# Kernel tuning notes

Hardware: AMD Instinct MI355X
Metric: run time of the kernel (lower is better)

Reference implementation:

```python
import jax, jax.numpy as jnp
import numpy as np
from jax import lax

D_MODEL = 512
D_STATE = 16
D_CONV = 4
DT_RANK = 32  # ceil(512/16)
BATCH = 4
SEQ = 2048
FN = 32


def setup_inputs() -> dict:
    key = jax.random.key(0)
    ks = jax.random.split(key, 12)
    s = 0.02
    d, n, r = D_MODEL, D_STATE, DT_RANK
    return {
        "atoms": jax.random.normal(ks[0], (BATCH, SEQ, d), jnp.float32),
        # normalized "adjacency"-like matrix so delta_p = dis_dense @ delta stays O(1)
        "dis_dense": jax.random.uniform(ks[1], (BATCH, SEQ, SEQ), jnp.float32) / SEQ,
        "gpt_emb": jax.random.normal(ks[2], (BATCH, d), jnp.float32),
        "fg_emb": jax.random.normal(ks[3], (BATCH, FN, d), jnp.float32),
        "in_proj_w": jax.random.normal(ks[4], (2 * d, d), jnp.float32) * s,
        "conv_w": jax.random.normal(ks[5], (d, 1, D_CONV), jnp.float32) * s,  # depthwise OIW
        "conv_b": jnp.zeros((d,), jnp.float32),
        "x_proj_w": jax.random.normal(ks[6], (r + 2 * n, d), jnp.float32) * s,
        "dt_proj_w": jax.random.normal(ks[7], (d, r), jnp.float32) * s,
        "dt_proj_b": jnp.full((d,), 0.5, jnp.float32),
        "A_log": jnp.log(jnp.broadcast_to(jnp.arange(1, n + 1, dtype=jnp.float32), (d, n))),
        "D_param": jnp.ones((d,), jnp.float32),
        "out_proj_w": jax.random.normal(ks[8], (d, d), jnp.float32) * s,
        "film_w1": jax.random.normal(ks[9], (d, d), jnp.float32) * s,
        "film_b1": jnp.zeros((d,), jnp.float32),
        "film_w2": jax.random.normal(ks[10], (2 * d, d), jnp.float32) * s,
        "film_b2": jnp.zeros((2 * d,), jnp.float32),
    }


def reference(atoms, dis_dense, gpt_emb, fg_emb,
              in_proj_w, conv_w, conv_b, x_proj_w, dt_proj_w, dt_proj_b,
              A_log, D_param, out_proj_w, film_w1, film_b1, film_w2, film_b2):
    b, l, d = atoms.shape
    n = A_log.shape[1]

    # --- CrossAttentionFusion: Q=atoms, K/V=fg_emb ---
    scores = jnp.einsum('bld,bfd->blf', atoms, fg_emb) / (d ** 0.5)
    attn = jax.nn.softmax(scores, axis=-1)
    x = atoms + jnp.einsum('blf,bfd->bld', attn, fg_emb)

    # --- FiLM modulation from gpt_emb ---
    h = jax.nn.silu(gpt_emb @ film_w1.T + film_b1)
    gamma, beta = jnp.split(h @ film_w2.T + film_b2, 2, axis=-1)
    x = x * gamma[:, None, :] + beta[:, None, :]

    # --- in_proj and split into (x, res) ---
    xs, res = jnp.split(x @ in_proj_w.T, 2, axis=-1)

    # --- depthwise causal-padded conv1d, truncate to l ---
    xc = jnp.transpose(xs, (0, 2, 1))  # [b, d, l]
    xc = lax.conv_general_dilated(xc, conv_w, window_strides=(1,),
                                  padding=[(D_CONV - 1, D_CONV - 1)],
                                  feature_group_count=d)[:, :, :l]
    xc = xc + conv_b[None, :, None]
    u = jax.nn.silu(jnp.transpose(xc, (0, 2, 1)))  # [b, l, d]

    # --- SSM ---
    A = -jnp.exp(A_log)                      # [d, n]
    x_dbl = u @ x_proj_w.T                   # [b, l, r+2n]
    delta, Bm, Cm = jnp.split(x_dbl, [DT_RANK, DT_RANK + n], axis=-1)
    delta = jax.nn.softplus(delta @ dt_proj_w.T + dt_proj_b)  # [b, l, d]
    delta_p = jnp.einsum('blk,bkd->bld', dis_dense, delta)     # graph-mixed delta

    deltaA = jnp.exp(delta_p[..., None] * A)                   # [b, l, d, n]
    deltaB_u = delta_p[..., None] * Bm[:, :, None, :] * u[..., None]  # [b, l, d, n]

    def step(carry, inp):
        dA_t, dBu_t, C_t = inp
        carry = dA_t * carry + dBu_t                # [b, d, n]
        y_t = jnp.einsum('bdn,bn->bd', carry, C_t)
        return carry, y_t

    init = jnp.zeros((b, d, n), deltaA.dtype)
    _, ys = lax.scan(step, init,
                     (jnp.moveaxis(deltaA, 1, 0),
                      jnp.moveaxis(deltaB_u, 1, 0),
                      jnp.moveaxis(Cm, 1, 0)))
    y = jnp.moveaxis(ys, 0, 1) + u * D_param       # [b, l, d]

    # --- gate, out_proj, nonfinite -> 0 ---
    y = y * jax.nn.silu(res)
    out = y @ out_proj_w.T
    return jnp.where(jnp.isfinite(out), out, 0.0)
```

## Files before the change

kernel.cpp:

```cpp
#include <hip/hip_runtime.h>
#include <stdint.h>

#define D_MODEL 512
#define D_STATE 16
#define DT_RANK 32
#define SEQ 2048
#define NBATCH 4
#define FN 32
#define CHUNK 16
#define NCHUNK 128
#define DPPLANE ((size_t)8192*D_MODEL)

typedef unsigned short u16;
using s16x8 = __attribute__((ext_vector_type(8))) short;
using f32x4 = __attribute__((ext_vector_type(4))) float;
using f32x8 = __attribute__((ext_vector_type(8))) float;
using bf16x8 = __attribute__((ext_vector_type(8))) __bf16;

typedef __attribute__((address_space(3))) void lds_void;
typedef __attribute__((address_space(1))) const void glb_void;

__device__ __forceinline__ void gload16(const void* g, void* l) {
  __builtin_amdgcn_global_load_lds((glb_void*)g, (lds_void*)l, 16, 0, 0);
}

__device__ inline u16 f2bf(float f) {
  uint32_t u = __float_as_uint(f);
  u += 0x7FFFu + ((u >> 16) & 1u);
  return (u16)(u >> 16);
}

__device__ __forceinline__ s16x8 pack8bf(float4 lo, float4 hi) {
  f32x8 v;
  v[0] = lo.x; v[1] = lo.y; v[2] = lo.z; v[3] = lo.w;
  v[4] = hi.x; v[5] = hi.y; v[6] = hi.z; v[7] = hi.w;
  bf16x8 b = __builtin_convertvector(v, bf16x8);
  return __builtin_bit_cast(s16x8, b);
}

__global__ __launch_bounds__(256) void film1_kernel(
    const float* __restrict__ gpt, const float* __restrict__ w1,
    const float* __restrict__ b1, float* __restrict__ h)
{
  int b = blockIdx.y, r0 = blockIdx.x*16, t = threadIdx.x;
  __shared__ float g[D_MODEL];
  for (int i = t; i < D_MODEL; i += 256) g[i] = gpt[b*D_MODEL + i];
  __syncthreads();
  int r = r0 + (t >> 4), ln = t & 15;
  const float* wr = &w1[(size_t)r*D_MODEL + ln*32];
  const float* gg = &g[ln*32];
  float s = 0.f;
  #pragma unroll
  for (int k = 0; k < 32; k += 4) {
    float4 w = *(const float4*)&wr[k];
    s += w.x*gg[k] + w.y*gg[k+1] + w.z*gg[k+2] + w.w*gg[k+3];
  }
  s += __shfl_down(s, 8); s += __shfl_down(s, 4);
  s += __shfl_down(s, 2); s += __shfl_down(s, 1);
  if (ln == 0) { float v = s + b1[r]; h[b*D_MODEL + r] = v / (1.f + expf(-v)); }
}

__global__ __launch_bounds__(256) void film2_kernel(
    const float* __restrict__ h, const float* __restrict__ w2,
    const float* __restrict__ b2, float* __restrict__ gb)
{
  int b = blockIdx.y, r0 = blockIdx.x*16, t = threadIdx.x;
  __shared__ float hs[D_MODEL];
  for (int i = t; i < D_MODEL; i += 256) hs[i] = h[b*D_MODEL + i];
  __syncthreads();
  int r = r0 + (t >> 4), ln = t & 15;
  const float* wr = &w2[(size_t)r*D_MODEL + ln*32];
  const float* gg = &hs[ln*32];
  float s = 0.f;
  #pragma unroll
  for (int k = 0; k < 32; k += 4) {
    float4 w = *(const float4*)&wr[k];
    s += w.x*gg[k] + w.y*gg[k+1] + w.z*gg[k+2] + w.w*gg[k+3];
  }
  s += __shfl_down(s, 8); s += __shfl_down(s, 4);
  s += __shfl_down(s, 2); s += __shfl_down(s, 1);
  if (ln == 0) gb[b*1024 + r] = s + b2[r];
}

__global__ __launch_bounds__(256) void build_fgpad_kernel(
    const float* __restrict__ fg, u16* __restrict__ fgpad)
{
  int row = blockIdx.x & 127, b = blockIdx.x >> 7, t = threadIdx.x;
  u16* dst = &fgpad[((size_t)b*128 + row)*D_MODEL];
  if (row < FN) {
    const float* src = &fg[((size_t)b*FN + row)*D_MODEL];
    float2 v = *(const float2*)&src[t*2];
    dst[t*2] = f2bf(v.x); dst[t*2+1] = f2bf(v.y);
  } else {
    dst[t*2] = 0; dst[t*2+1] = 0;
  }
}

__global__ __launch_bounds__(256) void softmax_kernel(
    const float* __restrict__ scores, float* __restrict__ attn)
{
  int wave = threadIdx.x >> 6, lane = threadIdx.x & 63;
  int row = blockIdx.x*4 + wave;
  float s = scores[(size_t)row*128 + (lane & 31)] * 0.04419417382415922f;
  float m = s;
  #pragma unroll
  for (int o = 16; o; o >>= 1) m = fmaxf(m, __shfl_xor(m, o));
  float e = __expf(s - m);
  float sum = e;
  #pragma unroll
  for (int o = 16; o; o >>= 1) sum += __shfl_xor(sum, o);
  if (lane < 32) attn[(size_t)row*FN + lane] = e / sum;
}

__global__ __launch_bounds__(256) void pv_film_kernel(
    const float* __restrict__ atoms, const float* __restrict__ fg,
    const float* __restrict__ attn, const float* __restrict__ gb,
    u16* __restrict__ xout)
{
  int wave = threadIdx.x >> 6, lane = threadIdx.x & 63;
  int row = blockIdx.x*4 + wave;
  int b = row >> 11;
  int d0 = lane*8;
  const float* arow = &atoms[(size_t)row*D_MODEL + d0];
  float4 acc0 = *(const float4*)&arow[0];
  float4 acc1 = *(const float4*)&arow[4];
  const float* attn_row = &attn[(size_t)row*FN];
  const float* fgb = &fg[(size_t)b*FN*D_MODEL + d0];
  #pragma unroll 8
  for (int f = 0; f < FN; f++) {
    float w = attn_row[f];
    float4 g0 = *(const float4*)&fgb[(size_t)f*D_MODEL];
    float4 g1 = *(const float4*)&fgb[(size_t)f*D_MODEL + 4];
    acc0.x += w*g0.x; acc0.y += w*g0.y; acc0.z += w*g0.z; acc0.w += w*g0.w;
    acc1.x += w*g1.x; acc1.y += w*g1.y; acc1.z += w*g1.z; acc1.w += w*g1.w;
  }
  const float* gbg = &gb[(size_t)b*1024 + d0];
  float4 gm0 = *(const float4*)&gbg[0];
  float4 gm1 = *(const float4*)&gbg[4];
  float4 bt0 = *(const float4*)&gbg[D_MODEL];
  float4 bt1 = *(const float4*)&gbg[D_MODEL + 4];
  s16x8 o;
  o[0] = (short)f2bf(acc0.x*gm0.x + bt0.x);
  o[1] = (short)f2bf(acc0.y*gm0.y + bt0.y);
  o[2] = (short)f2bf(acc0.z*gm0.z + bt0.z);
  o[3] = (short)f2bf(acc0.w*gm0.w + bt0.w);
  o[4] = (short)f2bf(acc1.x*gm1.x + bt1.x);
  o[5] = (short)f2bf(acc1.y*gm1.y + bt1.y);
  o[6] = (short)f2bf(acc1.z*gm1.z + bt1.z);
  o[7] = (short)f2bf(acc1.w*gm1.w + bt1.w);
  *(s16x8*)&xout[(size_t)row*D_MODEL + d0] = o;
}

__global__ __launch_bounds__(256) void cvt_bf16_kernel(
    const float* __restrict__ in, u16* __restrict__ out, int n4)
{
  int i = blockIdx.x*256 + threadIdx.x;
  if (i >= n4) return;
  float4 v = *(const float4*)&in[(size_t)i*4];
  ushort4 o; o.x = f2bf(v.x); o.y = f2bf(v.y); o.z = f2bf(v.z); o.w = f2bf(v.w);
  *(ushort4*)&out[(size_t)i*4] = o;
}

__global__ __launch_bounds__(256) void build_wcomb_kernel(
    const float* __restrict__ dtw, const float* __restrict__ xpw, u16* __restrict__ w)
{
  int row = blockIdx.x, t = threadIdx.x;
  if (row < D_MODEL) {
    __shared__ float dr[DT_RANK];
    if (t < DT_RANK) dr[t] = dtw[row*DT_RANK + t];
    __syncthreads();
    for (int k = t; k < D_MODEL; k += 256) {
      float s = 0.f;
      #pragma unroll
      for (int r = 0; r < DT_RANK; r++) s += dr[r] * xpw[r*D_MODEL + k];
      w[(size_t)row*D_MODEL + k] = f2bf(s);
    }
  } else if (row < D_MODEL + 32) {
    for (int k = t; k < D_MODEL; k += 256)
      w[(size_t)row*D_MODEL + k] = f2bf(xpw[(size_t)(DT_RANK + row - D_MODEL)*D_MODEL + k]);
  } else {
    for (int k = t; k < D_MODEL; k += 256)
      w[(size_t)row*D_MODEL + k] = 0;
  }
}

__global__ __launch_bounds__(256) void gemm_bt64_kernel(
    const u16* __restrict__ A, const u16* __restrict__ B, float* __restrict__ C,
    int M, int N, int K, int clampFinite)
{
  int gx = gridDim.x, gy = gridDim.y;
  int flat = blockIdx.x + gx*blockIdx.y;
  int cpx = (gx*gy) >> 3;
  flat = (flat & 7)*cpx + (flat >> 3);
  int bx = flat % gx, by = flat / gx;
  int m0 = by * 64, n0 = bx * 128;
  __shared__ u16 As[64][32];
  __shared__ u16 Bs[128][32];
  int tid = threadIdx.x, lane = tid & 63, wave = tid >> 6;
  int wm = (wave >> 1) * 32, wn = (wave & 1) * 64;
  int fr = lane & 15, fk = (lane >> 4) * 8;
  int srow = tid >> 2, scol = (tid & 3) * 8;
  f32x4 acc[2][4] = {};
  for (int k0 = 0; k0 < K; k0 += 32) {
    gload16(&A[(size_t)(m0 + srow)*K + k0 + scol],      &As[srow][scol]);
    gload16(&B[(size_t)(n0 + srow)*K + k0 + scol],      &Bs[srow][scol]);
    gload16(&B[(size_t)(n0 + 64 + srow)*K + k0 + scol], &Bs[64 + srow][scol]);
    __syncthreads();
    s16x8 af[2], bf[4];
    #pragma unroll
    for (int i = 0; i < 2; i++) af[i] = *(const s16x8*)(&As[wm + i*16 + fr][fk]);
    #pragma unroll
    for (int i = 0; i < 4; i++) bf[i] = *(const s16x8*)(&Bs[wn + i*16 + fr][fk]);
    #pragma unroll
    for (int mi = 0; mi < 2; mi++)
      #pragma unroll
      for (int ni = 0; ni < 4; ni++)
        acc[mi][ni] = __builtin_amdgcn_mfma_f32_16x16x32_bf16(af[mi], bf[ni], acc[mi][ni], 0, 0, 0);
    __syncthreads();
  }
  int cr = (lane >> 4) * 4, cc = lane & 15;
  #pragma unroll
  for (int mi = 0; mi < 2; mi++)
    #pragma unroll
    for (int ni = 0; ni < 4; ni++) {
      int rowb = m0 + wm + mi*16 + cr, col = n0 + wn + ni*16 + cc;
      #pragma unroll
      for (int r = 0; r < 4; r++) {
        float v = acc[mi][ni][r];
        if (clampFinite && !isfinite(v)) v = 0.f;
        C[(size_t)(rowb + r)*N + col] = v;
      }
    }
}

__global__ __launch_bounds__(256) void gemm_f32a_kernel(
    const float* __restrict__ Ag, const u16* __restrict__ Bg, float* __restrict__ Cg,
    int M, int N, int K, long long azs, long long bzs, long long czs,
    int clampFinite, int swz)
{
  int gx = gridDim.x, gy = gridDim.y;
  int flat = blockIdx.x + gx*(blockIdx.y + gy*blockIdx.z);
  if (swz) {
    int cpx = (gx*gy*(int)gridDim.z) >> 3;
    flat = (flat & 7)*cpx + (flat >> 3);
  }
  int bx = flat % gx, tmp = flat / gx;
  int by = tmp % gy, bz = tmp / gy;
  const float* A = Ag + (size_t)bz * azs;
  const u16* B = Bg + (size_t)bz * bzs;
  float* C = Cg + (size_t)bz * czs;
  int m0 = by * 128, n0 = bx * 128;
  __shared__ u16 As[128][32];
  __shared__ u16 Bs[128][32];
  int tid = threadIdx.x, lane = tid & 63, wave = tid >> 6;
  int wm = (wave >> 1) * 64, wn = (wave & 1) * 64;
  int fr = lane & 15, fk = (lane >> 4) * 8;
  int srow = tid >> 2, scol = (tid & 3) * 8;
  f32x4 acc[4][4] = {};
  for (int k0 = 0; k0 < K; k0 += 32) {
    const float* a0p = &A[(size_t)(m0 + srow)*K + k0 + scol];
    const float* a1p = &A[(size_t)(m0 + 64 + srow)*K + k0 + scol];
    float4 a00 = *(const float4*)&a0p[0];
    float4 a01 = *(const float4*)&a0p[4];
    float4 a10 = *(const float4*)&a1p[0];
    float4 a11 = *(const float4*)&a1p[4];
    gload16(&B[(size_t)(n0 + srow)*K + k0 + scol],      &Bs[srow][scol]);
    gload16(&B[(size_t)(n0 + 64 + srow)*K + k0 + scol], &Bs[64 + srow][scol]);
    *(s16x8*)&As[srow][scol]      = pack8bf(a00, a01);
    *(s16x8*)&As[64 + srow][scol] = pack8bf(a10, a11);
    __syncthreads();
    s16x8 af[4], bf[4];
    #pragma unroll
    for (int i = 0; i < 4; i++) af[i] = *(const s16x8*)(&As[wm + i*16 + fr][fk]);
    #pragma unroll
    for (int i = 0; i < 4; i++) bf[i] = *(const s16x8*)(&Bs[wn + i*16 + fr][fk]);
    #pragma unroll
    for (int mi = 0; mi < 4; mi++)
      #pragma unroll
      for (int ni = 0; ni < 4; ni++)
        acc[mi][ni] = __builtin_amdgcn_mfma_f32_16x16x32_bf16(af[mi], bf[ni], acc[mi][ni], 0, 0, 0);
    __syncthreads();
  }
  int cr = (lane >> 4) * 4, cc = lane & 15;
  #pragma unroll
  for (int mi = 0; mi < 4; mi++)
    #pragma unroll
    for (int ni = 0; ni < 4; ni++) {
      int rowb = m0 + wm + mi*16 + cr, col = n0 + wn + ni*16 + cc;
      #pragma unroll
      for (int r = 0; r < 4; r++) {
        float v = acc[mi][ni][r];
        if (clampFinite && !isfinite(v)) v = 0.f;
        C[(size_t)(rowb + r)*N + col] = v;
      }
    }
}

__global__ __launch_bounds__(256) void gemm_dp_splitk_kernel(
    const float* __restrict__ dis, const u16* __restrict__ deltaT,
    float* __restrict__ dpp)
{
  int gx = gridDim.x, gy = gridDim.y;
  int flat = blockIdx.x + gx*(blockIdx.y + gy*blockIdx.z);
  int cpx = (gx*gy*(int)gridDim.z) >> 3;
  flat = (flat & 7)*cpx + (flat >> 3);
  int bx = flat % gx, tmp = flat / gx;
  int by = tmp % gy, bz = tmp / gy;
  int b = bz >> 2, ks = bz & 3;
  const float* A = dis    + (size_t)b*SEQ*SEQ     + ks*512;
  const u16*  B = deltaT  + (size_t)b*D_MODEL*SEQ + ks*512;
  float*      C = dpp     + (size_t)ks*DPPLANE    + (size_t)b*SEQ*D_MODEL;
  int m0 = by * 128, n0 = bx * 128;
  __shared__ u16 As[128][32];
  __shared__ u16 Bs[128][32];
  int tid = threadIdx.x, lane = tid & 63, wave = tid >> 6;
  int wm = (wave >> 1) * 64, wn = (wave & 1) * 64;
  int fr = lane & 15, fk = (lane >> 4) * 8;
  int srow = tid >> 2, scol = (tid & 3) * 8;
  f32x4 acc[4][4] = {};
  for (int k0 = 0; k0 < 512; k0 += 32) {
    const float* a0p = &A[(size_t)(m0 + srow)*SEQ + k0 + scol];
    const float* a1p = &A[(size_t)(m0 + 64 + srow)*SEQ + k0 + scol];
    float4 a00 = *(const float4*)&a0p[0];
    float4 a01 = *(const float4*)&a0p[4];
    float4 a10 = *(const float4*)&a1p[0];
    float4 a11 = *(const float4*)&a1p[4];
    gload16(&B[(size_t)(n0 + srow)*SEQ + k0 + scol],      &Bs[srow][scol]);
    gload16(&B[(size_t)(n0 + 64 + srow)*SEQ + k0 + scol], &Bs[64 + srow][scol]);
    *(s16x8*)&As[srow][scol]      = pack8bf(a00, a01);
    *(s16x8*)&As[64 + srow][scol] = pack8bf(a10, a11);
    __syncthreads();
    s16x8 af[4], bf[4];
    #pragma unroll
    for (int i = 0; i < 4; i++) af[i] = *(const s16x8*)(&As[wm + i*16 + fr][fk]);
    #pragma unroll
    for (int i = 0; i < 4; i++) bf[i] = *(const s16x8*)(&Bs[wn + i*16 + fr][fk]);
    #pragma unroll
    for (int mi = 0; mi < 4; mi++)
      #pragma unroll
      for (int ni = 0; ni < 4; ni++)
        acc[mi][ni] = __builtin_amdgcn_mfma_f32_16x16x32_bf16(af[mi], bf[ni], acc[mi][ni], 0, 0, 0);
    __syncthreads();
  }
  int cr = (lane >> 4) * 4, cc = lane & 15;
  #pragma unroll
  for (int mi = 0; mi < 4; mi++)
    #pragma unroll
    for (int ni = 0; ni < 4; ni++) {
      int rowb = m0 + wm + mi*16 + cr, col = n0 + wn + ni*16 + cc;
      #pragma unroll
      for (int r = 0; r < 4; r++)
        C[(size_t)(rowb + r)*D_MODEL + col] = acc[mi][ni][r];
    }
}

__global__ __launch_bounds__(256) void gemm_delta_kernel(
    const u16* __restrict__ A, const u16* __restrict__ B,
    const float* __restrict__ dtb, u16* __restrict__ deltaT,
    float* __restrict__ Bv, float* __restrict__ Cv)
{
  int gx = gridDim.x, gy = gridDim.y;
  int flat = blockIdx.x + gx*blockIdx.y;
  int cpx = (gx*gy) >> 3;
  flat = (flat & 7)*cpx + (flat >> 3);
  int bx = flat % gx, by = flat / gx;
  int m0 = by * 64, n0 = bx * 128;
  __shared__ u16 As[64][32];
  __shared__ u16 Bs[128][32];
  int tid = threadIdx.x, lane = tid & 63, wave = tid >> 6;
  int wm = (wave >> 1) * 32, wn = (wave & 1) * 64;
  int fr = lane & 15, fk = (lane >> 4) * 8;
  int srow = tid >> 2, scol = (tid & 3) * 8;
  f32x4 acc[2][4] = {};
  for (int k0 = 0; k0 < D_MODEL; k0 += 32) {
    gload16(&A[(size_t)(m0 + srow)*D_MODEL + k0 + scol],      &As[srow][scol]);
    gload16(&B[(size_t)(n0 + srow)*D_MODEL + k0 + scol],      &Bs[srow][scol]);
    gload16(&B[(size_t)(n0 + 64 + srow)*D_MODEL + k0 + scol], &Bs[64 + srow][scol]);
    __syncthreads();
    s16x8 af[2], bf[4];
    #pragma unroll
    for (int i = 0; i < 2; i++) af[i] = *(const s16x8*)(&As[wm + i*16 + fr][fk]);
    #pragma unroll
    for (int i = 0; i < 4; i++) bf[i] = *(const s16x8*)(&Bs[wn + i*16 + fr][fk]);
    #pragma unroll
    for (int mi = 0; mi < 2; mi++)
      #pragma unroll
      for (int ni = 0; ni < 4; ni++)
        acc[mi][ni] = __builtin_amdgcn_mfma_f32_16x16x32_bf16(af[mi], bf[ni], acc[mi][ni], 0, 0, 0);
    __syncthreads();
  }
  int cr = (lane >> 4) * 4, cc = lane & 15;
  #pragma unroll
  for (int mi = 0; mi < 2; mi++)
    #pragma unroll
    for (int ni = 0; ni < 4; ni++) {
      int rowb = m0 + wm + mi*16 + cr, col = n0 + wn + ni*16 + cc;
      if (col < D_MODEL) {
        float bias = dtb[col];
        #pragma unroll
        for (int r = 0; r < 4; r++) {
          float v = acc[mi][ni][r] + bias;
          v = (v > 20.f) ? v : log1pf(expf(v));
          int gr = rowb + r;
          deltaT[((size_t)(gr >> 11)*D_MODEL + col)*SEQ + (gr & (SEQ-1))] = f2bf(v);
        }
      } else if (col < D_MODEL + 16) {
        #pragma unroll
        for (int r = 0; r < 4; r++)
          Bv[(size_t)(rowb + r)*D_STATE + (col - D_MODEL)] = acc[mi][ni][r];
      } else if (col < D_MODEL + 32) {
        #pragma unroll
        for (int r = 0; r < 4; r++)
          Cv[(size_t)(rowb + r)*D_STATE + (col - D_MODEL - 16)] = acc[mi][ni][r];
      }
    }
}

__global__ __launch_bounds__(256) void conv_silu_kernel(
    const float* __restrict__ xsres, const float* __restrict__ cw,
    const float* __restrict__ cb, float* __restrict__ u, u16* __restrict__ ubf)
{
  int idx = blockIdx.x*256 + threadIdx.x;
  int d = (idx & 127) * 4;
  int row = idx >> 7;
  int l = row & (SEQ - 1);
  float w[4][4];
  #pragma unroll
  for (int c = 0; c < 4; c++) *(float4*)w[c] = *(const float4*)&cw[(d + c)*4];
  float4 acc = *(const float4*)&cb[d];
  #pragma unroll
  for (int k = 0; k < 4; k++) {
    int li = l - 3 + k;
    if (li >= 0) {
      float4 v = *(const float4*)&xsres[(size_t)(row - 3 + k)*1024 + d];
      acc.x += v.x*w[0][k]; acc.y += v.y*w[1][k];
      acc.z += v.z*w[2][k]; acc.w += v.w*w[3][k];
    }
  }
  float4 o;
  o.x = acc.x/(1.f+expf(-acc.x)); o.y = acc.y/(1.f+expf(-acc.y));
  o.z = acc.z/(1.f+expf(-acc.z)); o.w = acc.w/(1.f+expf(-acc.w));
  *(float4*)&u[(size_t)row*D_MODEL + d] = o;
  ushort4 ob;
  ob.x = f2bf(o.x); ob.y = f2bf(o.y); ob.z = f2bf(o.z); ob.w = f2bf(o.w);
  *(ushort4*)&ubf[(size_t)row*D_MODEL + d] = ob;
}

__global__ __launch_bounds__(256) void scanA_kernel(
    float* __restrict__ dpp, const float* __restrict__ u,
    const float* __restrict__ Bv, const float* __restrict__ A_log,
    float* __restrict__ slocal, float* __restrict__ sumdp_out)
{
  int d = blockIdx.x*256 + threadIdx.x;
  int c = blockIdx.y, b = blockIdx.z;
  __shared__ float Bs[CHUNK][D_STATE];
  int t = threadIdx.x;
  size_t lbase = (size_t)b*SEQ + c*CHUNK;
  Bs[t >> 4][t & 15] = Bv[(lbase + (t >> 4))*D_STATE + (t & 15)];
  float a[D_STATE];
  #pragma unroll
  for (int n = 0; n < D_STATE; n += 4) {
    float4 v = *(const float4*)&A_log[(size_t)d*D_STATE + n];
    a[n] = -expf(v.x); a[n+1] = -expf(v.y); a[n+2] = -expf(v.z); a[n+3] = -expf(v.w);
  }
  __syncthreads();
  float s[D_STATE];
  #pragma unroll
  for (int n = 0; n < D_STATE; n++) s[n] = 0.f;
  float sd = 0.f;
  for (int j = 0; j < CHUNK; j++) {
    size_t r = lbase + j;
    size_t idx = r*D_MODEL + d;
    float dpv = dpp[idx] + dpp[idx + DPPLANE] + dpp[idx + 2*DPPLANE] + dpp[idx + 3*DPPLANE];
    dpp[idx] = dpv;
    float uv  = u[idx];
    sd += dpv;
    float dbu = dpv * uv;
    #pragma unroll
    for (int n = 0; n < D_STATE; n++)
      s[n] = __expf(a[n]*dpv)*s[n] + dbu*Bs[j][n];
  }
  size_t obase = ((size_t)b*NCHUNK + c)*D_MODEL + d;
  #pragma unroll
  for (int n = 0; n < D_STATE; n += 4)
    *(float4*)&slocal[obase*D_STATE + n] = make_float4(s[n], s[n+1], s[n+2], s[n+3]);
  sumdp_out[obase] = sd;
}

__global__ __launch_bounds__(256) void scanB_kernel(
    const float* __restrict__ slocal, const float* __restrict__ sumdp,
    const float* __restrict__ A_log, float* __restrict__ sIn)
{
  int g = blockIdx.x*256 + threadIdx.x;
  int n = g & 15, d = (g >> 4) & (D_MODEL - 1), b = g >> 13;
  float a = -expf(A_log[d*D_STATE + n]);
  float s = 0.f;
  for (int c = 0; c < NCHUNK; c++) {
    size_t idx = ((size_t)b*NCHUNK + c)*D_MODEL + d;
    sIn[idx*D_STATE + n] = s;
    s = __expf(a * sumdp[idx]) * s + slocal[idx*D_STATE + n];
  }
}

__global__ __launch_bounds__(256) void scanC_kernel(
    const float* __restrict__ dp, const float* __restrict__ u,
    const float* __restrict__ Bv, const float* __restrict__ Cv,
    const float* __restrict__ A_log, const float* __restrict__ Dp,
    const float* __restrict__ xsres, const float* __restrict__ sIn,
    u16* __restrict__ yout)
{
  int d = blockIdx.x*256 + threadIdx.x;
  int c = blockIdx.y, b = blockIdx.z;
  __shared__ float Bs[CHUNK][D_STATE];
  __shared__ float Cs[CHUNK][D_STATE];
  int t = threadIdx.x;
  size_t lbase = (size_t)b*SEQ + c*CHUNK;
  Bs[t >> 4][t & 15] = Bv[(lbase + (t >> 4))*D_STATE + (t & 15)];
  Cs[t >> 4][t & 15] = Cv[(lbase + (t >> 4))*D_STATE + (t & 15)];
  float a[D_STATE];
  #pragma unroll
  for (int n = 0; n < D_STATE; n += 4) {
    float4 v = *(const float4*)&A_log[(size_t)d*D_STATE + n];
    a[n] = -expf(v.x); a[n+1] = -expf(v.y); a[n+2] = -expf(v.z); a[n+3] = -expf(v.w);
  }
  float s[D_STATE];
  size_t ibase = (((size_t)b*NCHUNK + c)*D_MODEL + d)*D_STATE;
  #pragma unroll
  for (int n = 0; n < D_STATE; n += 4) {
    float4 v = *(const float4*)&sIn[ibase + n];
    s[n] = v.x; s[n+1] = v.y; s[n+2] = v.z; s[n+3] = v.w;
  }
  float dparam = Dp[d];
  __syncthreads();
  for (int j = 0; j < CHUNK; j++) {
    size_t r = lbase + j;
    float dpv = dp[r*D_MODEL + d];
    float uv  = u[r*D_MODEL + d];
    float dbu = dpv * uv;
    float y = 0.f;
    #pragma unroll
    for (int n = 0; n < D_STATE; n++) {
      s[n] = __expf(a[n]*dpv)*s[n] + dbu*Bs[j][n];
      y += s[n]*Cs[j][n];
    }
    y += uv * dparam;
    float rr = xsres[r*1024 + D_MODEL + d];
    y *= rr/(1.f + __expf(-rr));
    yout[r*D_MODEL + d] = f2bf(y);
  }
}

extern "C" void kernel_launch(void* const* d_in, const int* in_sizes, int n_in,
                              void* d_out, int out_size, void* d_ws, size_t ws_size,
                              hipStream_t stream)
{
  const float* atoms  = (const float*)d_in[0];
  const float* dis    = (const float*)d_in[1];
  const float* gpt    = (const float*)d_in[2];
  const float* fg     = (const float*)d_in[3];
  const float* inw    = (const float*)d_in[4];
  const float* convw  = (const float*)d_in[5];
  const float* convb  = (const float*)d_in[6];
  const float* xpw    = (const float*)d_in[7];
  const float* dtw    = (const float*)d_in[8];
  const float* dtb    = (const float*)d_in[9];
  const float* A_log  = (const float*)d_in[10];
  const float* Dparam = (const float*)d_in[11];
  const float* outw   = (const float*)d_in[12];
  const float* fw1    = (const float*)d_in[13];
  const float* fb1    = (const float*)d_in[14];
  const float* fw2    = (const float*)d_in[15];
  const float* fb2    = (const float*)d_in[16];

  char* ws = (char*)d_ws;
  size_t off = 0;
  auto alloc = [&](size_t bytes) { char* p = ws + off; off += (bytes + 255) & ~255ull; return p; };
  float* gb     = (float*)alloc((size_t)NBATCH*1024*4);
  float* hbuf   = (float*)alloc((size_t)NBATCH*512*4);
  float* attnb  = (float*)alloc((size_t)8192*FN*4);
  u16*   fgpad  = (u16*)  alloc((size_t)NBATCH*128*512*2);
  float* scores = (float*)alloc((size_t)NBATCH*2048*128*4);
  u16*   xbf    = (u16*)  alloc((size_t)8192*512*2);
  u16*   inwbf  = (u16*)  alloc((size_t)1024*512*2);
  u16*   outwbf = (u16*)  alloc((size_t)512*512*2);
  u16*   wcomb  = (u16*)  alloc((size_t)640*512*2);
  float* xsres  = (float*)alloc((size_t)8192*1024*4);
  float* dpp    = (float*)alloc(4*DPPLANE*4);
  float* ubuf   = (float*)alloc((size_t)8192*512*4);
  u16*   ubf    = (u16*)  alloc((size_t)8192*512*2);
  float* Bv     = (float*)alloc((size_t)8192*16*4);
  float* Cv     = (float*)alloc((size_t)8192*16*4);
  u16*   deltaT = (u16*)  alloc((size_t)NBATCH*512*2048*2);
  float* slocal = (float*)alloc((size_t)NBATCH*NCHUNK*512*16*4);
  float* sumdp  = (float*)alloc((size_t)NBATCH*NCHUNK*512*4);
  float* sIn    = (float*)alloc((size_t)NBATCH*NCHUNK*512*16*4);

  film1_kernel<<<dim3(32, NBATCH), 256, 0, stream>>>(gpt, fw1, fb1, hbuf);
  film2_kernel<<<dim3(64, NBATCH), 256, 0, stream>>>(hbuf, fw2, fb2, gb);

  build_fgpad_kernel<<<NBATCH*128, 256, 0, stream>>>(fg, fgpad);
  gemm_f32a_kernel<<<dim3(1, 2048/128, NBATCH), 256, 0, stream>>>(
      atoms, fgpad, scores, 2048, 128, 512,
      (long long)2048*512, (long long)128*512, (long long)2048*128, 0, 1);
  softmax_kernel<<<8192/4, 256, 0, stream>>>(scores, attnb);
  pv_film_kernel<<<8192/4, 256, 0, stream>>>(atoms, fg, attnb, gb, xbf);

  cvt_bf16_kernel<<<(1024*512/4)/256, 256, 0, stream>>>(inw, inwbf, 1024*512/4);
  cvt_bf16_kernel<<<(512*512/4)/256, 256, 0, stream>>>(outw, outwbf, 512*512/4);
  build_wcomb_kernel<<<640, 256, 0, stream>>>(dtw, xpw, wcomb);

  gemm_bt64_kernel<<<dim3(1024/128, 8192/64), 256, 0, stream>>>(
      xbf, inwbf, xsres, 8192, 1024, 512, 0);
  conv_silu_kernel<<<8192*128/256, 256, 0, stream>>>(xsres, convw, convb, ubuf, ubf);

  gemm_delta_kernel<<<dim3(640/128, 8192/64), 256, 0, stream>>>(
      ubf, wcomb, dtb, deltaT, Bv, Cv);

  gemm_dp_splitk_kernel<<<dim3(512/128, 2048/128, NBATCH*4), 256, 0, stream>>>(
      dis, deltaT, dpp);

  scanA_kernel<<<dim3(2, NCHUNK, NBATCH), 256, 0, stream>>>(dpp, ubuf, Bv, A_log, slocal, sumdp);
  scanB_kernel<<<32768/256, 256, 0, stream>>>(slocal, sumdp, A_log, sIn);
  u16* ybf = xbf;
  scanC_kernel<<<dim3(2, NCHUNK, NBATCH), 256, 0, stream>>>(dpp, ubuf, Bv, Cv, A_log, Dparam, xsres, sIn, ybf);

  gemm_bt64_kernel<<<dim3(512/128, 8192/64), 256, 0, stream>>>(
      ybf, outwbf, (float*)d_out, 8192, 512, 512, 1);
}
```

Measured before the change: 269.1 us.

## Double-buffer LDS tiles in bf16 GEMM and split-K delta GEMM kernels

Adds ping-pong shared-memory buffers to two GEMM kernels so the next K-tile is prefetched (via global_load_lds and register loads) while MFMAs run on the current tile. This removes one of the two barriers per iteration and overlaps global-load latency with compute. In exchange it doubles LDS use per block, which may reduce occupancy, and adds register pressure for the prefetched float4 values in the split-K kernel.

```diff
diff --git a/kernel.cpp b/kernel.cpp
--- a/kernel.cpp
+++ b/kernel.cpp
@@ -194,29 +194,41 @@
   flat = (flat & 7)*cpx + (flat >> 3);
   int bx = flat % gx, by = flat / gx;
   int m0 = by * 64, n0 = bx * 128;
-  __shared__ u16 As[64][32];
-  __shared__ u16 Bs[128][32];
+  __shared__ u16 As[2][64][32];
+  __shared__ u16 Bs[2][128][32];
   int tid = threadIdx.x, lane = tid & 63, wave = tid >> 6;
   int wm = (wave >> 1) * 32, wn = (wave & 1) * 64;
   int fr = lane & 15, fk = (lane >> 4) * 8;
   int srow = tid >> 2, scol = (tid & 3) * 8;
+  const u16* abase  = &A[(size_t)(m0 + srow)*K + scol];
+  const u16* b0base = &B[(size_t)(n0 + srow)*K + scol];
+  const u16* b1base = &B[(size_t)(n0 + 64 + srow)*K + scol];
+  gload16(abase,  &As[0][srow][scol]);
+  gload16(b0base, &Bs[0][srow][scol]);
+  gload16(b1base, &Bs[0][64 + srow][scol]);
+  __syncthreads();
   f32x4 acc[2][4] = {};
-  for (int k0 = 0; k0 < K; k0 += 32) {
-    gload16(&A[(size_t)(m0 + srow)*K + k0 + scol],      &As[srow][scol]);
-    gload16(&B[(size_t)(n0 + srow)*K + k0 + scol],      &Bs[srow][scol]);
-    gload16(&B[(size_t)(n0 + 64 + srow)*K + k0 + scol], &Bs[64 + srow][scol]);
-    __syncthreads();
+  int NT = K >> 5, cur = 0;
+  for (int t = 0; t < NT; t++) {
+    int nxt = cur ^ 1;
+    if (t + 1 < NT) {
+      int k0 = (t + 1) << 5;
+      gload16(&abase[k0],  &As[nxt][srow][scol]);
+      gload16(&b0base[k0], &Bs[nxt][srow][scol]);
+      gload16(&b1base[k0], &Bs[nxt][64 + srow][scol]);
+    }
     s16x8 af[2], bf[4];
     #pragma unroll
-    for (int i = 0; i < 2; i++) af[i] = *(const s16x8*)(&As[wm + i*16 + fr][fk]);
-    #pragma unroll
-    for (int i = 0; i < 4; i++) bf[i] = *(const s16x8*)(&Bs[wn + i*16 + fr][fk]);
+    for (int i = 0; i < 2; i++) af[i] = *(const s16x8*)(&As[cur][wm + i*16 + fr][fk]);
+    #pragma unroll
+    for (int i = 0; i < 4; i++) bf[i] = *(const s16x8*)(&Bs[cur][wn + i*16 + fr][fk]);
     #pragma unroll
     for (int mi = 0; mi < 2; mi++)
       #pragma unroll
       for (int ni = 0; ni < 4; ni++)
         acc[mi][ni] = __builtin_amdgcn_mfma_f32_16x16x32_bf16(af[mi], bf[ni], acc[mi][ni], 0, 0, 0);
     __syncthreads();
+    cur = nxt;
   }
   int cr = (lane >> 4) * 4, cc = lane & 15;
   #pragma unroll
@@ -311,36 +323,58 @@
   const u16*  B = deltaT  + (size_t)b*D_MODEL*SEQ + ks*512;
   float*      C = dpp     + (size_t)ks*DPPLANE    + (size_t)b*SEQ*D_MODEL;
   int m0 = by * 128, n0 = bx * 128;
-  __shared__ u16 As[128][32];
-  __shared__ u16 Bs[128][32];
+  __shared__ u16 As[2][128][32];
+  __shared__ u16 Bs[2][128][32];
   int tid = threadIdx.x, lane = tid & 63, wave = tid >> 6;
   int wm = (wave >> 1) * 64, wn = (wave & 1) * 64;
   int fr = lane & 15, fk = (lane >> 4) * 8;
   int srow = tid >> 2, scol = (tid & 3) * 8;
+  const float* a0base = &A[(size_t)(m0 + srow)*SEQ + scol];
+  const float* a1base = &A[(size_t)(m0 + 64 + srow)*SEQ + scol];
+  const u16* b0base = &B[(size_t)(n0 + srow)*SEQ + scol];
+  const u16* b1base = &B[(size_t)(n0 + 64 + srow)*SEQ + scol];
+  {
+    float4 a00 = *(const float4*)&a0base[0];
+    float4 a01 = *(const float4*)&a0base[4];
+    float4 a10 = *(const float4*)&a1base[0];
+    float4 a11 = *(const float4*)&a1base[4];
+    gload16(b0base, &Bs[0][srow][scol]);
+    gload16(b1base, &Bs[0][64 + srow][scol]);
+    *(s16x8*)&As[0][srow][scol]      = pack8bf(a00, a01);
+    *(s16x8*)&As[0][64 + srow][scol] = pack8bf(a10, a11);
+  }
+  __syncthreads();
   f32x4 acc[4][4] = {};
-  for (int k0 = 0; k0 < 512; k0 += 32) {
-    const float* a0p = &A[(size_t)(m0 + srow)*SEQ + k0 + scol];
-    const float* a1p = &A[(size_t)(m0 + 64 + srow)*SEQ + k0 + scol];
-    float4 a00 = *(const float4*)&a0p[0];
-    float4 a01 = *(const float4*)&a0p[4];
-    float4 a10 = *(const float4*)&a1p[0];
-    float4 a11 = *(const float4*)&a1p[4];
-    gload16(&B[(size_t)(n0 + srow)*SEQ + k0 + scol],      &Bs[srow][scol]);
-    gload16(&B[(size_t)(n0 + 64 + srow)*SEQ + k0 + scol], &Bs[64 + srow][scol]);
-    *(s16x8*)&As[srow][scol]      = pack8bf(a00, a01);
-    *(s16x8*)&As[64 + srow][scol] = pack8bf(a10, a11);
-    __syncthreads();
+  int cur = 0;
+  for (int t = 0; t < 16; t++) {
+    int nxt = cur ^ 1;
+    float4 n00, n01, n10, n11;
+    bool pf = (t + 1 < 16);
+    if (pf) {
+      int k0 = (t + 1) << 5;
+      n00 = *(const float4*)&a0base[k0];
+      n01 = *(const float4*)&a0base[k0 + 4];
+      n10 = *(const float4*)&a1base[k0];
+      n11 = *(const float4*)&a1base[k0 + 4];
+      gload16(&b0base[k0], &Bs[nxt][srow][scol]);
+      gload16(&b1base[k0], &Bs[nxt][64 + srow][scol]);
+    }
     s16x8 af[4], bf[4];
     #pragma unroll
-    for (int i = 0; i < 4; i++) af[i] = *(const s16x8*)(&As[wm + i*16 + fr][fk]);
-    #pragma unroll
-    for (int i = 0; i < 4; i++) bf[i] = *(const s16x8*)(&Bs[wn + i*16 + fr][fk]);
+    for (int i = 0; i < 4; i++) af[i] = *(const s16x8*)(&As[cur][wm + i*16 + fr][fk]);
+    #pragma unroll
+    for (int i = 0; i < 4; i++) bf[i] = *(const s16x8*)(&Bs[cur][wn + i*16 + fr][fk]);
     #pragma unroll
     for (int mi = 0; mi < 4; mi++)
       #pragma unroll
       for (int ni = 0; ni < 4; ni++)
         acc[mi][ni] = __builtin_amdgcn_mfma_f32_16x16x32_bf16(af[mi], bf[ni], acc[mi][ni], 0, 0, 0);
+    if (pf) {
+      *(s16x8*)&As[nxt][srow][scol]      = pack8bf(n00, n01);
+      *(s16x8*)&As[nxt][64 + srow][scol] = pack8bf(n10, n11);
+    }
     __syncthreads();
+    cur = nxt;
   }
   int cr = (lane >> 4) * 4, cc = lane & 15;
   #pragma unroll
```

New measurement: 266.7 us. About the same (-0.9%).

## Pre-convert dis matrix to bf16 and double-buffer LDS tiles in bt64 GEMM

Applied to the files above, without the earlier changes.

Adds a separate conversion pass that turns the fp32 dis_dense matrix into bf16, so the split-K delta-mixing GEMM can load both operands straight into LDS with async global-to-LDS loads instead of loading fp32 and packing in registers. The bf16 copy reuses the slocal scratch buffer, which is only about half the size needed, so it relies on the following sumdp and sIn allocations being contiguous and not yet in use. Separately, the bt64 GEMM gets double-buffered LDS tiles with a prologue load, so the next K-tile is fetched while MFMAs run on the current one. The conversion pass adds a full extra read and write of the large dis tensor, which may outweigh the cheaper GEMM loads.

```diff
diff --git a/kernel.cpp b/kernel.cpp
--- a/kernel.cpp
+++ b/kernel.cpp
@@ -194,29 +194,41 @@
   flat = (flat & 7)*cpx + (flat >> 3);
   int bx = flat % gx, by = flat / gx;
   int m0 = by * 64, n0 = bx * 128;
-  __shared__ u16 As[64][32];
-  __shared__ u16 Bs[128][32];
+  __shared__ u16 As[2][64][32];
+  __shared__ u16 Bs[2][128][32];
   int tid = threadIdx.x, lane = tid & 63, wave = tid >> 6;
   int wm = (wave >> 1) * 32, wn = (wave & 1) * 64;
   int fr = lane & 15, fk = (lane >> 4) * 8;
   int srow = tid >> 2, scol = (tid & 3) * 8;
+  const u16* abase  = &A[(size_t)(m0 + srow)*K + scol];
+  const u16* b0base = &B[(size_t)(n0 + srow)*K + scol];
+  const u16* b1base = &B[(size_t)(n0 + 64 + srow)*K + scol];
+  gload16(abase,  &As[0][srow][scol]);
+  gload16(b0base, &Bs[0][srow][scol]);
+  gload16(b1base, &Bs[0][64 + srow][scol]);
+  __syncthreads();
   f32x4 acc[2][4] = {};
-  for (int k0 = 0; k0 < K; k0 += 32) {
-    gload16(&A[(size_t)(m0 + srow)*K + k0 + scol],      &As[srow][scol]);
-    gload16(&B[(size_t)(n0 + srow)*K + k0 + scol],      &Bs[srow][scol]);
-    gload16(&B[(size_t)(n0 + 64 + srow)*K + k0 + scol], &Bs[64 + srow][scol]);
-    __syncthreads();
+  int NT = K >> 5, cur = 0;
+  for (int t = 0; t < NT; t++) {
+    int nxt = cur ^ 1;
+    if (t + 1 < NT) {
+      int k0 = (t + 1) << 5;
+      gload16(&abase[k0],  &As[nxt][srow][scol]);
+      gload16(&b0base[k0], &Bs[nxt][srow][scol]);
+      gload16(&b1base[k0], &Bs[nxt][64 + srow][scol]);
+    }
     s16x8 af[2], bf[4];
     #pragma unroll
-    for (int i = 0; i < 2; i++) af[i] = *(const s16x8*)(&As[wm + i*16 + fr][fk]);
-    #pragma unroll
-    for (int i = 0; i < 4; i++) bf[i] = *(const s16x8*)(&Bs[wn + i*16 + fr][fk]);
+    for (int i = 0; i < 2; i++) af[i] = *(const s16x8*)(&As[cur][wm + i*16 + fr][fk]);
+    #pragma unroll
+    for (int i = 0; i < 4; i++) bf[i] = *(const s16x8*)(&Bs[cur][wn + i*16 + fr][fk]);
     #pragma unroll
     for (int mi = 0; mi < 2; mi++)
       #pragma unroll
       for (int ni = 0; ni < 4; ni++)
         acc[mi][ni] = __builtin_amdgcn_mfma_f32_16x16x32_bf16(af[mi], bf[ni], acc[mi][ni], 0, 0, 0);
     __syncthreads();
+    cur = nxt;
   }
   int cr = (lane >> 4) * 4, cc = lane & 15;
   #pragma unroll
@@ -296,8 +308,8 @@
     }
 }
 
-__global__ __launch_bounds__(256) void gemm_dp_splitk_kernel(
-    const float* __restrict__ dis, const u16* __restrict__ deltaT,
+__global__ __launch_bounds__(256) void gemm_dpbf_splitk_kernel(
+    const u16* __restrict__ disbf, const u16* __restrict__ deltaT,
     float* __restrict__ dpp)
 {
   int gx = gridDim.x, gy = gridDim.y;
@@ -307,9 +319,9 @@
   int bx = flat % gx, tmp = flat / gx;
   int by = tmp % gy, bz = tmp / gy;
   int b = bz >> 2, ks = bz & 3;
-  const float* A = dis    + (size_t)b*SEQ*SEQ     + ks*512;
-  const u16*  B = deltaT  + (size_t)b*D_MODEL*SEQ + ks*512;
-  float*      C = dpp     + (size_t)ks*DPPLANE    + (size_t)b*SEQ*D_MODEL;
+  const u16* A = disbf  + (size_t)b*SEQ*SEQ     + ks*512;
+  const u16* B = deltaT + (size_t)b*D_MODEL*SEQ + ks*512;
+  float*     C = dpp    + (size_t)ks*DPPLANE    + (size_t)b*SEQ*D_MODEL;
   int m0 = by * 128, n0 = bx * 128;
   __shared__ u16 As[128][32];
   __shared__ u16 Bs[128][32];
@@ -319,16 +331,10 @@
   int srow = tid >> 2, scol = (tid & 3) * 8;
   f32x4 acc[4][4] = {};
   for (int k0 = 0; k0 < 512; k0 += 32) {
-    const float* a0p = &A[(size_t)(m0 + srow)*SEQ + k0 + scol];
-    const float* a1p = &A[(size_t)(m0 + 64 + srow)*SEQ + k0 + scol];
-    float4 a00 = *(const float4*)&a0p[0];
-    float4 a01 = *(const float4*)&a0p[4];
-    float4 a10 = *(const float4*)&a1p[0];
-    float4 a11 = *(const float4*)&a1p[4];
+    gload16(&A[(size_t)(m0 + srow)*SEQ + k0 + scol],      &As[srow][scol]);
+    gload16(&A[(size_t)(m0 + 64 + srow)*SEQ + k0 + scol], &As[64 + srow][scol]);
     gload16(&B[(size_t)(n0 + srow)*SEQ + k0 + scol],      &Bs[srow][scol]);
     gload16(&B[(size_t)(n0 + 64 + srow)*SEQ + k0 + scol], &Bs[64 + srow][scol]);
-    *(s16x8*)&As[srow][scol]      = pack8bf(a00, a01);
-    *(s16x8*)&As[64 + srow][scol] = pack8bf(a10, a11);
     __syncthreads();
     s16x8 af[4], bf[4];
     #pragma unroll
@@ -594,6 +600,7 @@
   float* slocal = (float*)alloc((size_t)NBATCH*NCHUNK*512*16*4);
   float* sumdp  = (float*)alloc((size_t)NBATCH*NCHUNK*512*4);
   float* sIn    = (float*)alloc((size_t)NBATCH*NCHUNK*512*16*4);
+  u16*   disbf  = (u16*)slocal;
 
   film1_kernel<<<dim3(32, NBATCH), 256, 0, stream>>>(gpt, fw1, fb1, hbuf);
   film2_kernel<<<dim3(64, NBATCH), 256, 0, stream>>>(hbuf, fw2, fb2, gb);
@@ -607,6 +614,7 @@
 
   cvt_bf16_kernel<<<(1024*512/4)/256, 256, 0, stream>>>(inw, inwbf, 1024*512/4);
   cvt_bf16_kernel<<<(512*512/4)/256, 256, 0, stream>>>(outw, outwbf, 512*512/4);
+  cvt_bf16_kernel<<<(NBATCH*2048*2048/4)/256, 256, 0, stream>>>(dis, disbf, NBATCH*2048*2048/4);
   build_wcomb_kernel<<<640, 256, 0, stream>>>(dtw, xpw, wcomb);
 
   gemm_bt64_kernel<<<dim3(1024/128, 8192/64), 256, 0, stream>>>(
@@ -616,8 +624,8 @@
   gemm_delta_kernel<<<dim3(640/128, 8192/64), 256, 0, stream>>>(
       ubf, wcomb, dtb, deltaT, Bv, Cv);
 
-  gemm_dp_splitk_kernel<<<dim3(512/128, 2048/128, NBATCH*4), 256, 0, stream>>>(
-      dis, deltaT, dpp);
+  gemm_dpbf_splitk_kernel<<<dim3(512/128, 2048/128, NBATCH*4), 256, 0, stream>>>(
+      disbf, deltaT, dpp);
 
   scanA_kernel<<<dim3(2, NCHUNK, NBATCH), 256, 0, stream>>>(dpp, ubuf, Bv, A_log, slocal, sumdp);
   scanB_kernel<<<32768/256, 256, 0, stream>>>(slocal, sumdp, A_log, sIn);
```

After: 262.3 us. -2.5%, faster.
